# Kernel tuning notes

Hardware: AMD Instinct MI355X
Metric: run time of the kernel (lower is better)

The kernel has to match this reference:

```python
import jax, jax.numpy as jnp
import numpy as np

KERNEL_SIZE = 4
SCALE = 0.5


def setup_inputs() -> dict:
    key = jax.random.key(0)
    k1, k2, k3 = jax.random.split(key, 3)
    M, K, N = 16384, 1024, 4096
    x = jax.random.normal(k1, (M, K), dtype=jnp.float32)
    weight = jax.random.normal(k2, (N, K), dtype=jnp.float32)
    bias = jax.random.normal(k3, (N,), dtype=jnp.float32)
    return {"x": x, "weight": weight, "bias": bias}


def reference(x, weight, bias):
    # y = x @ W^T + b : (M, N)
    y = jnp.einsum('mk,nk->mn', x, weight) + bias[None, :]
    M, N = y.shape
    valid_n = (N // KERNEL_SIZE) * KERNEL_SIZE
    # MaxPool1d(kernel_size, stride=kernel_size): (M, N//k, k) -> max over window
    pooled = jnp.max(y[:, :valid_n].reshape(M, valid_n // KERNEL_SIZE, KERNEL_SIZE), axis=-1)
    # sum over pooled features, then scale -> (M,)
    return jnp.sum(pooled, axis=-1) * SCALE
```

## Files before the change

kernel.cpp:

```cpp
#include <hip/hip_runtime.h>
#include <stdint.h>

#define M_DIM 16384
#define K_DIM 1024
#define N_DIM 4096
#define BM 128
#define BN 128
#define LDSP 40

#define TILE_ELEMS (128 * K_DIM)
#define SLAB_ELEMS (128 * 32)
#define CPAD 516

#define GBM 256
#define GBN 256
#define CHUNK 4096
#define BUFE  (8 * CHUNK)

typedef __bf16 bf16;
typedef __attribute__((ext_vector_type(8))) __bf16 bf16x8;
typedef __attribute__((ext_vector_type(4))) float f32x4;

__device__ __forceinline__ uint32_t pack2_bf16(float a, float b) {
    uint32_t ua = __float_as_uint(a);
    uint32_t ub = __float_as_uint(b);
    ua += 0x7fffu + ((ua >> 16) & 1u);
    ub += 0x7fffu + ((ub >> 16) & 1u);
    return (ua >> 16) | (ub & 0xffff0000u);
}

__global__ __launch_bounds__(256) void convert_pack_kernel(
    const float* __restrict__ x, const float* __restrict__ w,
    bf16* __restrict__ xp, bf16* __restrict__ wp, float* __restrict__ out)
{
    int g = blockIdx.x;
    const int t = threadIdx.x;
    if (g < (M_DIM / 256)) out[g * 256 + t] = 0.f;

    const float* src;
    bf16* dst;
    if (g < (M_DIM / 16)) {
        src = x + (size_t)g * 16 * K_DIM;  dst = xp;
    } else {
        g -= M_DIM / 16;
        src = w + (size_t)g * 16 * K_DIM;  dst = wp;
    }
    const int tile = g >> 3;
    const int rb   = g & 7;

    __shared__ uint32_t ls[16 * CPAD];

    #pragma unroll
    for (int i = 0; i < 16; ++i) {
        float4 v = ((const float4*)src)[i * 256 + t];
        uint2 d;
        d.x = pack2_bf16(v.x, v.y);
        d.y = pack2_bf16(v.z, v.w);
        *(uint2*)&ls[i * CPAD + t * 2] = d;
    }
    __syncthreads();

    const int wv = t >> 6, l = t & 63;
    const int lrow = l & 15, q = l >> 4;
    uint4* dst4 = (uint4*)(dst + (size_t)tile * TILE_ELEMS);
    #pragma unroll
    for (int it = 0; it < 8; ++it) {
        const int s = wv + it * 4;
        uint4 v = *(const uint4*)&ls[lrow * CPAD + s * 16 + q * 4];
        dst4[(s * 8 + rb) * 64 + l] = v;
    }
}


#define BARRIER() do { asm volatile("" ::: "memory"); \
                       __builtin_amdgcn_s_barrier();  \
                       asm volatile("" ::: "memory"); } while (0)
#define VMCNT4() asm volatile("s_waitcnt vmcnt(4)" ::: "memory")
#define VMCNT0() asm volatile("s_waitcnt vmcnt(0)" ::: "memory")

#define STAGE16(ldsOff, gsrc) \
    __builtin_amdgcn_global_load_lds( \
        (const __attribute__((address_space(1))) unsigned int*)(gsrc), \
        (__attribute__((address_space(3))) unsigned int*)&sm[(ldsOff) + w * 512], \
        16, 0, 0)

#define LDA4(sH, IB) do { \
    Af[0] = *(const bf16x8*)&sm[pO + (sH) * 8192 + aBase + ((IB) + 0) * 512]; \
    Af[1] = *(const bf16x8*)&sm[pO + (sH) * 8192 + aBase + ((IB) + 1) * 512]; \
    Af[2] = *(const bf16x8*)&sm[pO + (sH) * 8192 + aBase + ((IB) + 2) * 512]; \
    Af[3] = *(const bf16x8*)&sm[pO + (sH) * 8192 + aBase + ((IB) + 3) * 512]; \
} while (0)

#define LDB4(sH) do { \
    Bf[0] = *(const bf16x8*)&sm[pO + (sH) * 8192 + bBase + 0 * 512]; \
    Bf[1] = *(const bf16x8*)&sm[pO + (sH) * 8192 + bBase + 1 * 512]; \
    Bf[2] = *(const bf16x8*)&sm[pO + (sH) * 8192 + bBase + 2 * 512]; \
    Bf[3] = *(const bf16x8*)&sm[pO + (sH) * 8192 + bBase + 3 * 512]; \
} while (0)

#define MFMA16(IB) do { \
    __builtin_amdgcn_s_setprio(1); \
    _Pragma("unroll") \
    for (int ii = 0; ii < 4; ++ii) \
        _Pragma("unroll") \
        for (int jj = 0; jj < 4; ++jj) \
            acc[(IB) + ii][jj] = __builtin_amdgcn_mfma_f32_16x16x32_bf16( \
                Af[ii], Bf[jj], acc[(IB) + ii][jj], 0, 0, 0); \
    __builtin_amdgcn_s_setprio(0); \
} while (0)

#define TILE_BODY(T, P, STG) do { \
    const int pO  = (P) * BUFE; \
    const int pnO = ((P) ^ 1) * BUFE; \
     \
    LDA4(0, 0); LDB4(0); \
    if (STG) { STAGE16(pnO + 0 * CHUNK, Ag + 0 * TILE_ELEMS + (size_t)(2 * (T) + 2) * CHUNK + toff); \
               STAGE16(pnO + 1 * CHUNK, Ag + 1 * TILE_ELEMS + (size_t)(2 * (T) + 2) * CHUNK + toff); } \
    BARRIER(); MFMA16(0); BARRIER(); \
     \
    LDA4(0, 4); \
    if (STG) { STAGE16(pnO + 4 * CHUNK, Bg + 0 * TILE_ELEMS + (size_t)(2 * (T) + 2) * CHUNK + toff); \
               STAGE16(pnO + 5 * CHUNK, Bg + 1 * TILE_ELEMS + (size_t)(2 * (T) + 2) * CHUNK + toff); } \
    BARRIER(); MFMA16(4); \
    if (STG) { VMCNT4(); } else { VMCNT0(); }    \
    BARRIER(); \
     \
    LDA4(1, 0); LDB4(1); \
    if (STG) { STAGE16(pnO + 2 * CHUNK, Ag + 0 * TILE_ELEMS + (size_t)(2 * (T) + 3) * CHUNK + toff); \
               STAGE16(pnO + 3 * CHUNK, Ag + 1 * TILE_ELEMS + (size_t)(2 * (T) + 3) * CHUNK + toff); } \
    BARRIER(); MFMA16(0); BARRIER(); \
     \
    LDA4(1, 4); \
    if (STG) { STAGE16(pnO + 6 * CHUNK, Bg + 0 * TILE_ELEMS + (size_t)(2 * (T) + 3) * CHUNK + toff); \
               STAGE16(pnO + 7 * CHUNK, Bg + 1 * TILE_ELEMS + (size_t)(2 * (T) + 3) * CHUNK + toff); } \
    BARRIER(); MFMA16(4); \
    if (STG) { VMCNT4(); }                        \
    BARRIER(); \
} while (0)

__global__ __launch_bounds__(512, 2) void gemm_pool_8phase_kernel(
    const bf16* __restrict__ xp, const bf16* __restrict__ wp,
    const float* __restrict__ bias, float* __restrict__ out)
{
    __shared__ bf16 sm[2 * BUFE];

    const int b  = blockIdx.x;
    const int bx = b & (N_DIM / GBN - 1);
    const int by = b >> 4;

    const int tid  = threadIdx.x;
    const int lane = tid & 63;
    const int w    = tid >> 6;
    const int wm   = w >> 2;
    const int wn   = w & 3;
    const int lr   = lane & 15;
    const int quad = lane >> 4;
    const int toff = tid * 8;

    const bf16* __restrict__ Ag = xp + (size_t)(2 * by) * TILE_ELEMS;
    const bf16* __restrict__ Bg = wp + (size_t)(2 * bx) * TILE_ELEMS;

    const int aBase = wm * CHUNK + lane * 8;
    const int bBase = 4 * CHUNK + (wn >> 1) * CHUNK + (wn & 1) * 2048 + lane * 8;

    f32x4 acc[8][4] = {};
    bf16x8 Af[4], Bf[4];

    STAGE16(0 * CHUNK, Ag + 0 * TILE_ELEMS + toff);
    STAGE16(1 * CHUNK, Ag + 1 * TILE_ELEMS + toff);
    STAGE16(4 * CHUNK, Bg + 0 * TILE_ELEMS + toff);
    STAGE16(5 * CHUNK, Bg + 1 * TILE_ELEMS + toff);
    STAGE16(2 * CHUNK, Ag + 0 * TILE_ELEMS + CHUNK + toff);
    STAGE16(3 * CHUNK, Ag + 1 * TILE_ELEMS + CHUNK + toff);
    STAGE16(6 * CHUNK, Bg + 0 * TILE_ELEMS + CHUNK + toff);
    STAGE16(7 * CHUNK, Bg + 1 * TILE_ELEMS + CHUNK + toff);
    VMCNT4(); BARRIER();

    #pragma unroll
    for (int t = 0; t < 15; ++t) {
        const int p = t & 1;
        TILE_BODY(t, p, 1);
    }
    TILE_BODY(15, 1, 0);

    float bv[4];
    #pragma unroll
    for (int j = 0; j < 4; ++j)
        bv[j] = bias[bx * GBN + wn * 64 + j * 16 + lr];

    #pragma unroll
    for (int i = 0; i < 8; ++i) {
        float rs[4] = {0.f, 0.f, 0.f, 0.f};
        #pragma unroll
        for (int j = 0; j < 4; ++j) {
            #pragma unroll
            for (int r = 0; r < 4; ++r) {
                float v = acc[i][j][r] + bv[j];
                v = fmaxf(v, __shfl_xor(v, 1, 64));
                v = fmaxf(v, __shfl_xor(v, 2, 64));
                rs[r] += v;
            }
        }
        #pragma unroll
        for (int r = 0; r < 4; ++r) {
            rs[r] += __shfl_xor(rs[r], 4, 64);
            rs[r] += __shfl_xor(rs[r], 8, 64);
        }
        if (lr == 0) {
            const int row = by * GBM + wm * 128 + i * 16 + quad * 4;
            #pragma unroll
            for (int r = 0; r < 4; ++r)
                atomicAdd(&out[row + r], rs[r] * 0.5f);
        }
    }
}

__global__ __launch_bounds__(256) void fused_linear_pool_kernel(
    const float* __restrict__ x, const float* __restrict__ wt,
    const float* __restrict__ bias, float* __restrict__ out)
{
    __shared__ uint32_t sA[BM * LDSP / 2];
    __shared__ uint32_t sB[BN * LDSP / 2];

    const int tid = threadIdx.x;
    const int bx = blockIdx.x;
    const int by = blockIdx.y;

    const float* Abase = x  + (size_t)by * BM * K_DIM;
    const float* Bbase = wt + (size_t)bx * BN * K_DIM;

    const int lane = tid & 63;
    const int wave = tid >> 6;
    const int wm = wave >> 1;
    const int wn = wave & 1;
    const int lr = lane & 15;
    const int quad = lane >> 4;

    const int srow  = tid >> 2;
    const int scol  = (tid & 3) * 8;
    const int swidx = (tid & 3) * 4;

    f32x4 acc[4][4] = {};

    for (int kt = 0; kt < K_DIM; kt += 32) {
        #pragma unroll
        for (int p = 0; p < 2; ++p) {
            const int r = srow + p * 64;
            const float4* ga = (const float4*)(Abase + (size_t)r * K_DIM + kt + scol);
            const float4* gb = (const float4*)(Bbase + (size_t)r * K_DIM + kt + scol);
            float4 a0 = ga[0], a1 = ga[1], b0 = gb[0], b1 = gb[1];
            uint4 wa;
            wa.x = pack2_bf16(a0.x, a0.y); wa.y = pack2_bf16(a0.z, a0.w);
            wa.z = pack2_bf16(a1.x, a1.y); wa.w = pack2_bf16(a1.z, a1.w);
            *(uint4*)&sA[r * (LDSP / 2) + swidx] = wa;
            uint4 wbv;
            wbv.x = pack2_bf16(b0.x, b0.y); wbv.y = pack2_bf16(b0.z, b0.w);
            wbv.z = pack2_bf16(b1.x, b1.y); wbv.w = pack2_bf16(b1.z, b1.w);
            *(uint4*)&sB[r * (LDSP / 2) + swidx] = wbv;
        }
        __syncthreads();

        bf16x8 af[4], bfr[4];
        #pragma unroll
        for (int i = 0; i < 4; ++i)
            af[i] = *(const bf16x8*)((const bf16*)sA + (wm * 64 + i * 16 + lr) * LDSP + quad * 8);
        #pragma unroll
        for (int j = 0; j < 4; ++j)
            bfr[j] = *(const bf16x8*)((const bf16*)sB + (wn * 64 + j * 16 + lr) * LDSP + quad * 8);

        #pragma unroll
        for (int i = 0; i < 4; ++i)
            #pragma unroll
            for (int j = 0; j < 4; ++j)
                acc[i][j] = __builtin_amdgcn_mfma_f32_16x16x32_bf16(af[i], bfr[j], acc[i][j], 0, 0, 0);
        __syncthreads();
    }

    float bv[4];
    #pragma unroll
    for (int j = 0; j < 4; ++j)
        bv[j] = bias[bx * BN + wn * 64 + j * 16 + lr];

    #pragma unroll
    for (int i = 0; i < 4; ++i) {
        float rsum[4] = {0.f, 0.f, 0.f, 0.f};
        #pragma unroll
        for (int j = 0; j < 4; ++j) {
            #pragma unroll
            for (int r = 0; r < 4; ++r) {
                float t = acc[i][j][r] + bv[j];
                t = fmaxf(t, __shfl_xor(t, 1, 64));
                t = fmaxf(t, __shfl_xor(t, 2, 64));
                t += __shfl_xor(t, 4, 64);
                t += __shfl_xor(t, 8, 64);
                rsum[r] += t;
            }
        }
        if (lr == 0) {
            const int row = by * BM + wm * 64 + i * 16 + quad * 4;
            #pragma unroll
            for (int r = 0; r < 4; ++r)
                atomicAdd(&out[row + r], rsum[r] * 0.5f);
        }
    }
}

extern "C" void kernel_launch(void* const* d_in, const int* in_sizes, int n_in,
                              void* d_out, int out_size, void* d_ws, size_t ws_size,
                              hipStream_t stream) {
    const float* x  = (const float*)d_in[0];
    const float* wt = (const float*)d_in[1];
    const float* bs = (const float*)d_in[2];
    float* out = (float*)d_out;

    const size_t xe = (size_t)M_DIM * K_DIM;
    const size_t we = (size_t)N_DIM * K_DIM;
    const size_t need = (xe + we) * sizeof(bf16);

    if (ws_size >= need) {
        bf16* xp = (bf16*)d_ws;
        bf16* wp = xp + xe;
        const int nconv = (M_DIM / 16) + (N_DIM / 16);
        convert_pack_kernel<<<nconv, 256, 0, stream>>>(x, wt, xp, wp, out);
        gemm_pool_8phase_kernel<<<(M_DIM / GBM) * (N_DIM / GBN), 512, 0, stream>>>(xp, wp, bs, out);
    } else {
        hipMemsetAsync(out, 0, (size_t)out_size * sizeof(float), stream);
        dim3 grid(N_DIM / BN, M_DIM / BM);
        fused_linear_pool_kernel<<<grid, 256, 0, stream>>>(x, wt, bs, out);
    }
}
```

Baseline: 246.9 us.

## Replace double-buffered GEMM pipeline with 4-slot LDS ring and register prefetch

Restructures the main bf16 GEMM loop from a two-buffer, eight-phase schedule into a 4-slot LDS ring over 32 K-slabs. Global-to-LDS loads run two slabs ahead, and the next slab's A-low and B fragments are read into alternating register sets while the current MFMAs run. This leaves one barrier per slab instead of several per tile. The aim is to overlap LDS reads, global staging and MFMA work more tightly and cut synchronization stalls, at the cost of extra fragment registers that may pressure occupancy at two blocks per CU.

Result: no change. 243.7 us, median of 2 (-1.3%).

```diff
diff --git a/kernel.cpp b/kernel.cpp
--- a/kernel.cpp
+++ b/kernel.cpp
@@ -9,13 +9,12 @@
 #define LDSP 40
 
 #define TILE_ELEMS (128 * K_DIM)
-#define SLAB_ELEMS (128 * 32)
 #define CPAD 516
 
 #define GBM 256
 #define GBN 256
-#define CHUNK 4096
-#define BUFE  (8 * CHUNK)
+#define NSLAB 32
+#define SLOT_E 16384
 
 typedef __bf16 bf16;
 typedef __attribute__((ext_vector_type(8))) __bf16 bf16x8;
@@ -72,77 +71,59 @@
 }
 
 
-#define BARRIER() do { asm volatile("" ::: "memory"); \
-                       __builtin_amdgcn_s_barrier();  \
-                       asm volatile("" ::: "memory"); } while (0)
+#define BAR() do { asm volatile("" ::: "memory"); \
+                   __builtin_amdgcn_s_barrier();  \
+                   asm volatile("" ::: "memory"); } while (0)
 #define VMCNT4() asm volatile("s_waitcnt vmcnt(4)" ::: "memory")
 #define VMCNT0() asm volatile("s_waitcnt vmcnt(0)" ::: "memory")
 
-#define STAGE16(ldsOff, gsrc) \
+#define STG(sl, ch, gsrc) \
     __builtin_amdgcn_global_load_lds( \
         (const __attribute__((address_space(1))) unsigned int*)(gsrc), \
-        (__attribute__((address_space(3))) unsigned int*)&sm[(ldsOff) + w * 512], \
+        (__attribute__((address_space(3))) unsigned int*)&sm[(((sl) & 3) * SLOT_E) + (ch) * 4096 + w * 512], \
         16, 0, 0)
 
-#define LDA4(sH, IB) do { \
-    Af[0] = *(const bf16x8*)&sm[pO + (sH) * 8192 + aBase + ((IB) + 0) * 512]; \
-    Af[1] = *(const bf16x8*)&sm[pO + (sH) * 8192 + aBase + ((IB) + 1) * 512]; \
-    Af[2] = *(const bf16x8*)&sm[pO + (sH) * 8192 + aBase + ((IB) + 2) * 512]; \
-    Af[3] = *(const bf16x8*)&sm[pO + (sH) * 8192 + aBase + ((IB) + 3) * 512]; \
+#define STG_A(t) do { STG(t, 0, Ag + (size_t)(t) * 4096 + toff); \
+                      STG(t, 1, Ag + TILE_ELEMS + (size_t)(t) * 4096 + toff); } while (0)
+#define STG_B(t) do { STG(t, 2, Bg + (size_t)(t) * 4096 + toff); \
+                      STG(t, 3, Bg + TILE_ELEMS + (size_t)(t) * 4096 + toff); } while (0)
+
+#define RD4(dst, base) do { \
+    _Pragma("unroll") \
+    for (int _i = 0; _i < 4; ++_i) \
+        dst[_i] = *(const bf16x8*)&sm[(base) + _i * 512]; \
 } while (0)
 
-#define LDB4(sH) do { \
-    Bf[0] = *(const bf16x8*)&sm[pO + (sH) * 8192 + bBase + 0 * 512]; \
-    Bf[1] = *(const bf16x8*)&sm[pO + (sH) * 8192 + bBase + 1 * 512]; \
-    Bf[2] = *(const bf16x8*)&sm[pO + (sH) * 8192 + bBase + 2 * 512]; \
-    Bf[3] = *(const bf16x8*)&sm[pO + (sH) * 8192 + bBase + 3 * 512]; \
-} while (0)
-
-#define MFMA16(IB) do { \
+#define MFMA16X(Aset, Bset, IB) do { \
     __builtin_amdgcn_s_setprio(1); \
     _Pragma("unroll") \
     for (int ii = 0; ii < 4; ++ii) \
         _Pragma("unroll") \
         for (int jj = 0; jj < 4; ++jj) \
             acc[(IB) + ii][jj] = __builtin_amdgcn_mfma_f32_16x16x32_bf16( \
-                Af[ii], Bf[jj], acc[(IB) + ii][jj], 0, 0, 0); \
+                Aset[ii], Bset[jj], acc[(IB) + ii][jj], 0, 0, 0); \
     __builtin_amdgcn_s_setprio(0); \
 } while (0)
 
-#define TILE_BODY(T, P, STG) do { \
-    const int pO  = (P) * BUFE; \
-    const int pnO = ((P) ^ 1) * BUFE; \
-     \
-    LDA4(0, 0); LDB4(0); \
-    if (STG) { STAGE16(pnO + 0 * CHUNK, Ag + 0 * TILE_ELEMS + (size_t)(2 * (T) + 2) * CHUNK + toff); \
-               STAGE16(pnO + 1 * CHUNK, Ag + 1 * TILE_ELEMS + (size_t)(2 * (T) + 2) * CHUNK + toff); } \
-    BARRIER(); MFMA16(0); BARRIER(); \
-     \
-    LDA4(0, 4); \
-    if (STG) { STAGE16(pnO + 4 * CHUNK, Bg + 0 * TILE_ELEMS + (size_t)(2 * (T) + 2) * CHUNK + toff); \
-               STAGE16(pnO + 5 * CHUNK, Bg + 1 * TILE_ELEMS + (size_t)(2 * (T) + 2) * CHUNK + toff); } \
-    BARRIER(); MFMA16(4); \
-    if (STG) { VMCNT4(); } else { VMCNT0(); }    \
-    BARRIER(); \
-     \
-    LDA4(1, 0); LDB4(1); \
-    if (STG) { STAGE16(pnO + 2 * CHUNK, Ag + 0 * TILE_ELEMS + (size_t)(2 * (T) + 3) * CHUNK + toff); \
-               STAGE16(pnO + 3 * CHUNK, Ag + 1 * TILE_ELEMS + (size_t)(2 * (T) + 3) * CHUNK + toff); } \
-    BARRIER(); MFMA16(0); BARRIER(); \
-     \
-    LDA4(1, 4); \
-    if (STG) { STAGE16(pnO + 6 * CHUNK, Bg + 0 * TILE_ELEMS + (size_t)(2 * (T) + 3) * CHUNK + toff); \
-               STAGE16(pnO + 7 * CHUNK, Bg + 1 * TILE_ELEMS + (size_t)(2 * (T) + 3) * CHUNK + toff); } \
-    BARRIER(); MFMA16(4); \
-    if (STG) { VMCNT4(); }                        \
-    BARRIER(); \
+#define SLAB(s, CUR, NXT) do { \
+    if ((s) + 2 < NSLAB) STG_A((s) + 2); \
+    RD4(Ahi, (((s) & 3) * SLOT_E) + aOff + 2048); \
+    MFMA16X(Alo##CUR, Bv##CUR, 0); \
+    if ((s) + 2 < NSLAB) STG_B((s) + 2); \
+    if ((s) == NSLAB - 2) { VMCNT0(); } else if ((s) < NSLAB - 2) { VMCNT4(); } \
+    BAR(); \
+    if ((s) + 1 < NSLAB) { \
+        RD4(Alo##NXT, ((((s) + 1) & 3) * SLOT_E) + aOff); \
+        RD4(Bv##NXT,  ((((s) + 1) & 3) * SLOT_E) + bOff); \
+    } \
+    MFMA16X(Ahi, Bv##CUR, 4); \
 } while (0)
 
-__global__ __launch_bounds__(512, 2) void gemm_pool_8phase_kernel(
+__global__ __launch_bounds__(512, 2) void gemm_pool_ring_kernel(
     const bf16* __restrict__ xp, const bf16* __restrict__ wp,
     const float* __restrict__ bias, float* __restrict__ out)
 {
-    __shared__ bf16 sm[2 * BUFE];
+    __shared__ bf16 sm[4 * SLOT_E];
 
     const int b  = blockIdx.x;
     const int bx = b & (N_DIM / GBN - 1);
@@ -160,28 +141,23 @@
     const bf16* __restrict__ Ag = xp + (size_t)(2 * by) * TILE_ELEMS;
     const bf16* __restrict__ Bg = wp + (size_t)(2 * bx) * TILE_ELEMS;
 
-    const int aBase = wm * CHUNK + lane * 8;
-    const int bBase = 4 * CHUNK + (wn >> 1) * CHUNK + (wn & 1) * 2048 + lane * 8;
+    const int aOff = wm * 4096 + lane * 8;
+    const int bOff = 8192 + (wn >> 1) * 4096 + (wn & 1) * 2048 + lane * 8;
 
     f32x4 acc[8][4] = {};
-    bf16x8 Af[4], Bf[4];
-
-    STAGE16(0 * CHUNK, Ag + 0 * TILE_ELEMS + toff);
-    STAGE16(1 * CHUNK, Ag + 1 * TILE_ELEMS + toff);
-    STAGE16(4 * CHUNK, Bg + 0 * TILE_ELEMS + toff);
-    STAGE16(5 * CHUNK, Bg + 1 * TILE_ELEMS + toff);
-    STAGE16(2 * CHUNK, Ag + 0 * TILE_ELEMS + CHUNK + toff);
-    STAGE16(3 * CHUNK, Ag + 1 * TILE_ELEMS + CHUNK + toff);
-    STAGE16(6 * CHUNK, Bg + 0 * TILE_ELEMS + CHUNK + toff);
-    STAGE16(7 * CHUNK, Bg + 1 * TILE_ELEMS + CHUNK + toff);
-    VMCNT4(); BARRIER();
-
-    #pragma unroll
-    for (int t = 0; t < 15; ++t) {
-        const int p = t & 1;
-        TILE_BODY(t, p, 1);
-    }
-    TILE_BODY(15, 1, 0);
+    bf16x8 AloA[4], AloB[4], Ahi[4], BvA[4], BvB[4];
+
+    STG_A(0); STG_B(0);
+    STG_A(1); STG_B(1);
+    VMCNT4(); BAR();
+    RD4(AloA, aOff);
+    RD4(BvA,  bOff);
+
+    #pragma unroll
+    for (int sp = 0; sp < NSLAB / 2; ++sp) {
+        SLAB(2 * sp,     A, B);
+        SLAB(2 * sp + 1, B, A);
+    }
 
     float bv[4];
     #pragma unroll
@@ -322,7 +298,7 @@
         bf16* wp = xp + xe;
         const int nconv = (M_DIM / 16) + (N_DIM / 16);
         convert_pack_kernel<<<nconv, 256, 0, stream>>>(x, wt, xp, wp, out);
-        gemm_pool_8phase_kernel<<<(M_DIM / GBM) * (N_DIM / GBN), 512, 0, stream>>>(xp, wp, bs, out);
+        gemm_pool_ring_kernel<<<(M_DIM / GBM) * (N_DIM / GBN), 512, 0, stream>>>(xp, wp, bs, out);
     } else {
         hipMemsetAsync(out, 0, (size_t)out_size * sizeof(float), stream);
         dim3 grid(N_DIM / BN, M_DIM / BM);
```
